# Optimization experiments

Hardware: AMD Instinct MI355X
Metric: run time of the kernel (lower is better)

The kernel has to match this reference:

```python
import jax, jax.numpy as jnp
import numpy as np

EPSILON = 1e-8
DT = 0.1
STEPS = 3
MASK_DENSITY = 0.01


def setup_inputs() -> dict:
    key = jax.random.key(0)
    k1, k2 = jax.random.split(key)
    B, S, D = 4, 4096, 2
    psi = jax.random.normal(k1, (B, S, D), dtype=jnp.float32)
    # binary mask: threshold a uniform draw to get a sparse 0/1 adjacency
    u = jax.random.uniform(k2, (B, S, S), dtype=jnp.float32)
    binary_mask = (u < MASK_DENSITY).astype(jnp.float32)
    return {"psi": psi, "binary_mask": binary_mask}


def reference(psi, binary_mask):
    def force(state):
        # adjacency-weighted aggregation minus self: [B,S,S] @ [B,S,2]
        return jnp.einsum('bij,bjd->bid', binary_mask, state) - state

    def step(p, _):
        r = jnp.linalg.norm(p, axis=-1, keepdims=True)          # [B,S,1]
        k1 = force(p)
        psi_star = p + DT * k1
        star_norm = jnp.linalg.norm(psi_star, axis=-1, keepdims=True)
        psi_star = psi_star * (r / (star_norm + EPSILON))       # renormalize to r
        k2 = force(psi_star)
        p_new = p + 0.5 * DT * (k1 + k2)
        new_norm = jnp.linalg.norm(p_new, axis=-1, keepdims=True)
        p_new = p_new * (r / (new_norm + EPSILON))              # norm-preserving
        return p_new, None

    psi_out, _ = jax.lax.scan(step, psi, None, length=STEPS)
    return psi_out
```

## Files before the change

kernel.cpp:

```cpp
#include <hip/hip_runtime.h>
#include <stdint.h>

#define BATCH   4
#define SEQ     4096
#define NROWS   (BATCH * SEQ)
#define SLOTS   80
#define SENT    SEQ
#define DTS     0.1f
#define HALF_DT 0.05f
#define EPS     1e-8f

#define NBLK    256
#define NTHR    1024

typedef float fx4 __attribute__((ext_vector_type(4)));

__device__ __forceinline__ float2 ballot_force_sum(unsigned long long w,
                                                   const float2* __restrict__ gb,
                                                   int lane) {
    const int colbase = ((lane >> 2) << 8) | (lane & 3);
    float sx = 0.f, sy = 0.f;
    while (w) {
        int j = __builtin_ctzll(w);
        w &= (w - 1);
        float2 v = gb[colbase + (j << 2)];
        sx += v.x; sy += v.y;
    }
#pragma unroll
    for (int m = 32; m >= 1; m >>= 1) {
        sx += __shfl_xor(sx, m, 64);
        sy += __shfl_xor(sy, m, 64);
    }
    return make_float2(sx, sy);
}

__global__ __launch_bounds__(256)
void compress_phaseA(const float* __restrict__ mask,
                     const float2* __restrict__ psi,
                     ushort* __restrict__ idx,
                     float2* __restrict__ k1buf,
                     float2* __restrict__ starbuf,
                     float*  __restrict__ rbuf) {
    const int row  = (blockIdx.x * blockDim.x + threadIdx.x) >> 6;
    const int lane = threadIdx.x & 63;

    const fx4* src = reinterpret_cast<const fx4*>(mask + (size_t)row * SEQ);
    unsigned long long word = 0ull;
#pragma unroll
    for (int c = 0; c < 16; ++c) {
        fx4 v = __builtin_nontemporal_load(&src[c * 64 + lane]);
        unsigned long long b;
        b = __ballot(v.x != 0.f); if (lane == c * 4 + 0) word = b;
        b = __ballot(v.y != 0.f); if (lane == c * 4 + 1) word = b;
        b = __ballot(v.z != 0.f); if (lane == c * 4 + 2) word = b;
        b = __ballot(v.w != 0.f); if (lane == c * 4 + 3) word = b;
    }

    int pc  = __popcll(word);
    int inc = pc;
#pragma unroll
    for (int ofs = 1; ofs < 64; ofs <<= 1) {
        int t = __shfl_up(inc, ofs, 64);
        if (lane >= ofs) inc += t;
    }
    int pos   = inc - pc;
    int total = __shfl(inc, 63, 64);

    ushort* dst = idx + (size_t)row * SLOTS;
    const int colbase = ((lane >> 2) << 8) | (lane & 3);
    unsigned long long w = word;
    while (w) {
        int j = __builtin_ctzll(w);
        w &= (w - 1);
        if (pos < SLOTS) dst[pos] = (ushort)(colbase + (j << 2));
        ++pos;
    }
    for (int s = total + lane; s < SLOTS; s += 64) dst[s] = (ushort)SENT;

    const int bidx = row >> 12;
    float2 sum = ballot_force_sum(word, psi + ((size_t)bidx << 12), lane);
    float2 p  = psi[row];
    float r   = sqrtf(p.x * p.x + p.y * p.y);
    float k1x = sum.x - p.x, k1y = sum.y - p.y;
    float tx  = p.x + DTS * k1x, ty = p.y + DTS * k1y;
    float sc  = r / (sqrtf(tx * tx + ty * ty) + EPS);
    if (lane == 0) {
        k1buf[row]   = make_float2(k1x, k1y);
        rbuf[row]    = r;
        starbuf[row] = make_float2(tx * sc, ty * sc);
    }
}

__device__ __forceinline__ void gbar(int* __restrict__ bar, int gen) {
    __syncthreads();
    if (threadIdx.x == 0) {
        __threadfence();
        atomicAdd(bar, 1);
        while (__hip_atomic_load(bar, __ATOMIC_RELAXED,
                                 __HIP_MEMORY_SCOPE_AGENT) < gen * NBLK)
            __builtin_amdgcn_s_sleep(2);
        __threadfence();
    }
    __syncthreads();
}

__global__ __launch_bounds__(NTHR)
void forces(const ushort* __restrict__ idx,
            const float2* __restrict__ psi,
            float2* __restrict__ pbuf,
            float2* __restrict__ star,
            float2* __restrict__ k1buf,
            float*  __restrict__ rbuf,
            float2* __restrict__ out,
            int*    __restrict__ bar) {
    __shared__ float2 SRC[SEQ + 2];

    const int t    = threadIdx.x;
    const int g    = t >> 4;
    const int q    = t & 15;
    const int row  = (blockIdx.x << 6) + g;
    const int bidx = row >> 12;
    const int rloc = row & 4095;
    const size_t bo = (size_t)bidx << 12;

    const ushort* __restrict__ ip = idx + (size_t)row * SLOTS;
    int c[5];
#pragma unroll
    for (int r = 0; r < 5; ++r) c[r] = ip[q * 5 + r];

    int gen = 0;
#pragma unroll 1
    for (int ph = 0; ph < 5; ++ph) {
        const bool isA = (ph & 1);
        const float2* __restrict__ gb = (isA ? pbuf : star) + bo;

        {
            const float4* __restrict__ s4 = reinterpret_cast<const float4*>(gb);
            float4* l4 = reinterpret_cast<float4*>(SRC);
            l4[t] = s4[t];
            l4[t + 1024] = s4[t + 1024];
            if (t == 0) SRC[SEQ] = make_float2(0.f, 0.f);
        }
        float2 p = make_float2(0.f, 0.f), k1 = make_float2(0.f, 0.f);
        float  rv = 0.f;
        if (!isA) {
            p  = (ph == 0) ? psi[row] : pbuf[row];
            k1 = k1buf[row];
            rv = rbuf[row];
        }
        __syncthreads();

        float sx = 0.f, sy = 0.f;
#pragma unroll
        for (int r = 0; r < 5; ++r) {
            float2 v = SRC[c[r]];
            sx += v.x; sy += v.y;
        }
#pragma unroll
        for (int m = 8; m >= 1; m >>= 1) {
            sx += __shfl_xor(sx, m, 64);
            sy += __shfl_xor(sy, m, 64);
        }

        if (q == 0) {
            if (isA) {
                float2 ps = SRC[rloc];
                float r   = sqrtf(ps.x * ps.x + ps.y * ps.y);
                float k1x = sx - ps.x, k1y = sy - ps.y;
                float tx  = ps.x + DTS * k1x, ty = ps.y + DTS * k1y;
                float sc  = r / (sqrtf(tx * tx + ty * ty) + EPS);
                k1buf[row] = make_float2(k1x, k1y);
                rbuf[row]  = r;
                star[row]  = make_float2(tx * sc, ty * sc);
            } else {
                float2 st = SRC[rloc];
                float k2x = sx - st.x, k2y = sy - st.y;
                float nx  = p.x + HALF_DT * (k1.x + k2x);
                float ny  = p.y + HALF_DT * (k1.y + k2y);
                float sc  = rv / (sqrtf(nx * nx + ny * ny) + EPS);
                float2 pn = make_float2(nx * sc, ny * sc);
                if (ph == 4) out[row]  = pn;
                else         pbuf[row] = pn;
            }
        }
        if (ph < 4) gbar(bar, ++gen);
    }
}

extern "C" void kernel_launch(void* const* d_in, const int* in_sizes, int n_in,
                              void* d_out, int out_size, void* d_ws, size_t ws_size,
                              hipStream_t stream) {
    const float* psi  = (const float*)d_in[0];
    const float* mask = (const float*)d_in[1];
    float2* out2 = (float2*)d_out;

    char* ws = (char*)d_ws;
    ushort* idx  = (ushort*)ws;
    float2* pbuf = (float2*)(ws + (size_t)NROWS * SLOTS * sizeof(ushort));
    float2* star = pbuf + NROWS;
    float2* k1   = star + NROWS;
    float*  rbuf = (float*)(k1 + NROWS);
    int*    bar  = (int*)(rbuf + NROWS);

    const float2* psi2 = (const float2*)psi;

    hipMemsetAsync(bar, 0, 64, stream);
    compress_phaseA<<<NROWS / 4, 256, 0, stream>>>(mask, psi2, idx, k1, star, rbuf);
    forces<<<NBLK, NTHR, 0, stream>>>(idx, psi2, pbuf, star, k1, rbuf, out2, bar);
}
```

Measured before the change: 406.9 us.

## Replace persistent grid-barrier kernel with per-phase kernel launches

Replaces the single persistent 256x1024 kernel that used a software grid barrier between five phases with five separate launches of a templated 256-thread kernel, each handling 64 rows (4 rows per 16-lane group). Stream ordering now provides the inter-phase sync instead of atomic spinning, and the barrier memset goes away. In exchange each launch pays launch overhead and reloads the 32KB gather source into LDS per block. Phase 1 reads and writes pbuf in place, which is safe because each row only reads and writes its own entry.

Result: faster. 356.5 us (-12.4%).

```diff
diff --git a/kernel.cpp b/kernel.cpp
--- a/kernel.cpp
+++ b/kernel.cpp
@@ -9,9 +9,6 @@
 #define DTS     0.1f
 #define HALF_DT 0.05f
 #define EPS     1e-8f
-
-#define NBLK    256
-#define NTHR    1024
 
 typedef float fx4 __attribute__((ext_vector_type(4)));
 
@@ -91,69 +88,59 @@
     }
 }
 
-__device__ __forceinline__ void gbar(int* __restrict__ bar, int gen) {
-    __syncthreads();
-    if (threadIdx.x == 0) {
-        __threadfence();
-        atomicAdd(bar, 1);
-        while (__hip_atomic_load(bar, __ATOMIC_RELAXED,
-                                 __HIP_MEMORY_SCOPE_AGENT) < gen * NBLK)
-            __builtin_amdgcn_s_sleep(2);
-        __threadfence();
-    }
-    __syncthreads();
-}
-
-__global__ __launch_bounds__(NTHR)
-void forces(const ushort* __restrict__ idx,
-            const float2* __restrict__ psi,
-            float2* __restrict__ pbuf,
-            float2* __restrict__ star,
-            float2* __restrict__ k1buf,
-            float*  __restrict__ rbuf,
-            float2* __restrict__ out,
-            int*    __restrict__ bar) {
+template <int PHASE>
+__global__ __launch_bounds__(256)
+void force_step(const ushort* __restrict__ idx,
+                const float2* __restrict__ pIn,
+                const float2* __restrict__ gath,
+                float2* __restrict__ k1buf,
+                float*  __restrict__ rbuf,
+                float2* __restrict__ outbuf) {
     __shared__ float2 SRC[SEQ + 2];
 
-    const int t    = threadIdx.x;
-    const int g    = t >> 4;
-    const int q    = t & 15;
-    const int row  = (blockIdx.x << 6) + g;
-    const int bidx = row >> 12;
-    const int rloc = row & 4095;
+    const int t     = threadIdx.x;
+    const int g     = t >> 4;
+    const int q     = t & 15;
+    const int row0  = (blockIdx.x << 6);
+    const int bidx  = row0 >> 12;
     const size_t bo = (size_t)bidx << 12;
+    const float2* __restrict__ gb = gath + bo;
 
-    const ushort* __restrict__ ip = idx + (size_t)row * SLOTS;
-    int c[5];
+    {
+        const float4* __restrict__ s4 = reinterpret_cast<const float4*>(gb);
+        float4* l4 = reinterpret_cast<float4*>(SRC);
 #pragma unroll
-    for (int r = 0; r < 5; ++r) c[r] = ip[q * 5 + r];
+        for (int k = 0; k < 8; ++k) l4[t + k * 256] = s4[t + k * 256];
+        if (t == 0) SRC[SEQ] = make_float2(0.f, 0.f);
+    }
 
-    int gen = 0;
-#pragma unroll 1
-    for (int ph = 0; ph < 5; ++ph) {
-        const bool isA = (ph & 1);
-        const float2* __restrict__ gb = (isA ? pbuf : star) + bo;
+    int c[4][5];
+    float2 p[4], k1[4];
+    float  rv[4];
+#pragma unroll
+    for (int rr = 0; rr < 4; ++rr) {
+        const int row = row0 + g + (rr << 4);
+        const ushort* __restrict__ ip = idx + (size_t)row * SLOTS;
+#pragma unroll
+        for (int r = 0; r < 5; ++r) c[rr][r] = ip[q * 5 + r];
+        if (PHASE == 1) {
+            p[rr]  = pIn[row];
+            k1[rr] = k1buf[row];
+            rv[rr] = rbuf[row];
+        }
+    }
 
-        {
-            const float4* __restrict__ s4 = reinterpret_cast<const float4*>(gb);
-            float4* l4 = reinterpret_cast<float4*>(SRC);
-            l4[t] = s4[t];
-            l4[t + 1024] = s4[t + 1024];
-            if (t == 0) SRC[SEQ] = make_float2(0.f, 0.f);
-        }
-        float2 p = make_float2(0.f, 0.f), k1 = make_float2(0.f, 0.f);
-        float  rv = 0.f;
-        if (!isA) {
-            p  = (ph == 0) ? psi[row] : pbuf[row];
-            k1 = k1buf[row];
-            rv = rbuf[row];
-        }
-        __syncthreads();
+    __syncthreads();
+
+#pragma unroll
+    for (int rr = 0; rr < 4; ++rr) {
+        const int row  = row0 + g + (rr << 4);
+        const int rloc = row & 4095;
 
         float sx = 0.f, sy = 0.f;
 #pragma unroll
         for (int r = 0; r < 5; ++r) {
-            float2 v = SRC[c[r]];
+            float2 v = SRC[c[rr][r]];
             sx += v.x; sy += v.y;
         }
 #pragma unroll
@@ -163,27 +150,24 @@
         }
 
         if (q == 0) {
-            if (isA) {
+            if (PHASE == 0) {
                 float2 ps = SRC[rloc];
                 float r   = sqrtf(ps.x * ps.x + ps.y * ps.y);
                 float k1x = sx - ps.x, k1y = sy - ps.y;
                 float tx  = ps.x + DTS * k1x, ty = ps.y + DTS * k1y;
                 float sc  = r / (sqrtf(tx * tx + ty * ty) + EPS);
-                k1buf[row] = make_float2(k1x, k1y);
-                rbuf[row]  = r;
-                star[row]  = make_float2(tx * sc, ty * sc);
+                k1buf[row]  = make_float2(k1x, k1y);
+                rbuf[row]   = r;
+                outbuf[row] = make_float2(tx * sc, ty * sc);
             } else {
                 float2 st = SRC[rloc];
                 float k2x = sx - st.x, k2y = sy - st.y;
-                float nx  = p.x + HALF_DT * (k1.x + k2x);
-                float ny  = p.y + HALF_DT * (k1.y + k2y);
-                float sc  = rv / (sqrtf(nx * nx + ny * ny) + EPS);
-                float2 pn = make_float2(nx * sc, ny * sc);
-                if (ph == 4) out[row]  = pn;
-                else         pbuf[row] = pn;
+                float nx  = p[rr].x + HALF_DT * (k1[rr].x + k2x);
+                float ny  = p[rr].y + HALF_DT * (k1[rr].y + k2y);
+                float sc  = rv[rr] / (sqrtf(nx * nx + ny * ny) + EPS);
+                outbuf[row] = make_float2(nx * sc, ny * sc);
             }
         }
-        if (ph < 4) gbar(bar, ++gen);
     }
 }
 
@@ -200,11 +184,14 @@
     float2* star = pbuf + NROWS;
     float2* k1   = star + NROWS;
     float*  rbuf = (float*)(k1 + NROWS);
-    int*    bar  = (int*)(rbuf + NROWS);
 
     const float2* psi2 = (const float2*)psi;
+    const int gridF = NROWS / 64;
 
-    hipMemsetAsync(bar, 0, 64, stream);
     compress_phaseA<<<NROWS / 4, 256, 0, stream>>>(mask, psi2, idx, k1, star, rbuf);
-    forces<<<NBLK, NTHR, 0, stream>>>(idx, psi2, pbuf, star, k1, rbuf, out2, bar);
+    force_step<1><<<gridF, 256, 0, stream>>>(idx, psi2, star, k1, rbuf, pbuf);
+    force_step<0><<<gridF, 256, 0, stream>>>(idx, nullptr, pbuf, k1, rbuf, star);
+    force_step<1><<<gridF, 256, 0, stream>>>(idx, pbuf, star, k1, rbuf, pbuf);
+    force_step<0><<<gridF, 256, 0, stream>>>(idx, nullptr, pbuf, k1, rbuf, star);
+    force_step<1><<<gridF, 256, 0, stream>>>(idx, pbuf, star, k1, rbuf, out2);
 }
```

## Shrink forces blocks to 256 threads and use relaxed-atomic fence-free grid barrier

Applied to the files above, without the earlier changes.

Rewrites the persistent forces kernel to use 256-thread blocks, each thread processing four rows, and replaces the fenced grid barrier with a relaxed atomic counter without threadfences. Cross-block shared state (star, pbuf) is now read and written through agent-scope relaxed atomic 64-bit loads and stores, so it stays coherent without full fences. The aim is to cut barrier cost between phases and reduce per-block overhead, at the risk of subtle memory-ordering issues and a longer per-thread LDS fill.

After: 376.8 us. 7.4% less time.

```diff
diff --git a/kernel.cpp b/kernel.cpp
--- a/kernel.cpp
+++ b/kernel.cpp
@@ -11,9 +11,31 @@
 #define EPS     1e-8f
 
 #define NBLK    256
-#define NTHR    1024
 
 typedef float fx4 __attribute__((ext_vector_type(4)));
+
+__device__ __forceinline__ float2 aload8(const float2* p) {
+    unsigned long long u = __hip_atomic_load(
+        reinterpret_cast<const unsigned long long*>(p),
+        __ATOMIC_RELAXED, __HIP_MEMORY_SCOPE_AGENT);
+    float2 f; __builtin_memcpy(&f, &u, 8); return f;
+}
+__device__ __forceinline__ void astore8(float2* p, float2 v) {
+    unsigned long long u; __builtin_memcpy(&u, &v, 8);
+    __hip_atomic_store(reinterpret_cast<unsigned long long*>(p), u,
+                       __ATOMIC_RELAXED, __HIP_MEMORY_SCOPE_AGENT);
+}
+
+__device__ __forceinline__ void gbar(int* bar, int target) {
+    __syncthreads();
+    if (threadIdx.x == 0) {
+        __hip_atomic_fetch_add(bar, 1, __ATOMIC_RELAXED, __HIP_MEMORY_SCOPE_AGENT);
+        while (__hip_atomic_load(bar, __ATOMIC_RELAXED,
+                                 __HIP_MEMORY_SCOPE_AGENT) < target)
+            __builtin_amdgcn_s_sleep(4);
+    }
+    __syncthreads();
+}
 
 __device__ __forceinline__ float2 ballot_force_sum(unsigned long long w,
                                                    const float2* __restrict__ gb,
@@ -91,20 +113,7 @@
     }
 }
 
-__device__ __forceinline__ void gbar(int* __restrict__ bar, int gen) {
-    __syncthreads();
-    if (threadIdx.x == 0) {
-        __threadfence();
-        atomicAdd(bar, 1);
-        while (__hip_atomic_load(bar, __ATOMIC_RELAXED,
-                                 __HIP_MEMORY_SCOPE_AGENT) < gen * NBLK)
-            __builtin_amdgcn_s_sleep(2);
-        __threadfence();
-    }
-    __syncthreads();
-}
-
-__global__ __launch_bounds__(NTHR)
+__global__ __launch_bounds__(256)
 void forces(const ushort* __restrict__ idx,
             const float2* __restrict__ psi,
             float2* __restrict__ pbuf,
@@ -118,72 +127,86 @@
     const int t    = threadIdx.x;
     const int g    = t >> 4;
     const int q    = t & 15;
-    const int row  = (blockIdx.x << 6) + g;
-    const int bidx = row >> 12;
-    const int rloc = row & 4095;
+    const int row0 = (blockIdx.x << 6);
+    const int bidx = row0 >> 12;
     const size_t bo = (size_t)bidx << 12;
 
-    const ushort* __restrict__ ip = idx + (size_t)row * SLOTS;
-    int c[5];
-#pragma unroll
-    for (int r = 0; r < 5; ++r) c[r] = ip[q * 5 + r];
-
-    int gen = 0;
+    int c[4][5];
+#pragma unroll
+    for (int rr = 0; rr < 4; ++rr) {
+        const int row = row0 + g + (rr << 4);
+        const ushort* __restrict__ ip = idx + (size_t)row * SLOTS;
+#pragma unroll
+        for (int r = 0; r < 5; ++r) c[rr][r] = ip[q * 5 + r];
+    }
+
 #pragma unroll 1
     for (int ph = 0; ph < 5; ++ph) {
         const bool isA = (ph & 1);
-        const float2* __restrict__ gb = (isA ? pbuf : star) + bo;
+        const float2* gbG = (isA ? pbuf : star) + bo;
 
         {
-            const float4* __restrict__ s4 = reinterpret_cast<const float4*>(gb);
-            float4* l4 = reinterpret_cast<float4*>(SRC);
-            l4[t] = s4[t];
-            l4[t + 1024] = s4[t + 1024];
+            float2 v[16];
+#pragma unroll
+            for (int k = 0; k < 16; ++k) v[k] = aload8(gbG + t + k * 256);
+#pragma unroll
+            for (int k = 0; k < 16; ++k) SRC[t + k * 256] = v[k];
             if (t == 0) SRC[SEQ] = make_float2(0.f, 0.f);
         }
-        float2 p = make_float2(0.f, 0.f), k1 = make_float2(0.f, 0.f);
-        float  rv = 0.f;
+
+        float2 p[4], k1v[4];
+        float  rv[4];
         if (!isA) {
-            p  = (ph == 0) ? psi[row] : pbuf[row];
-            k1 = k1buf[row];
-            rv = rbuf[row];
+#pragma unroll
+            for (int rr = 0; rr < 4; ++rr) {
+                const int row = row0 + g + (rr << 4);
+                p[rr]   = (ph == 0) ? psi[row] : aload8(&pbuf[row]);
+                k1v[rr] = k1buf[row];
+                rv[rr]  = rbuf[row];
+            }
         }
         __syncthreads();
 
-        float sx = 0.f, sy = 0.f;
-#pragma unroll
-        for (int r = 0; r < 5; ++r) {
-            float2 v = SRC[c[r]];
-            sx += v.x; sy += v.y;
+#pragma unroll
+        for (int rr = 0; rr < 4; ++rr) {
+            const int row  = row0 + g + (rr << 4);
+            const int rloc = row & 4095;
+
+            float sx = 0.f, sy = 0.f;
+#pragma unroll
+            for (int r = 0; r < 5; ++r) {
+                float2 v = SRC[c[rr][r]];
+                sx += v.x; sy += v.y;
+            }
+#pragma unroll
+            for (int m = 8; m >= 1; m >>= 1) {
+                sx += __shfl_xor(sx, m, 64);
+                sy += __shfl_xor(sy, m, 64);
+            }
+
+            if (q == 0) {
+                if (isA) {
+                    float2 ps = SRC[rloc];
+                    float r   = sqrtf(ps.x * ps.x + ps.y * ps.y);
+                    float k1x = sx - ps.x, k1y = sy - ps.y;
+                    float tx  = ps.x + DTS * k1x, ty = ps.y + DTS * k1y;
+                    float sc  = r / (sqrtf(tx * tx + ty * ty) + EPS);
+                    k1buf[row] = make_float2(k1x, k1y);
+                    rbuf[row]  = r;
+                    astore8(&star[row], make_float2(tx * sc, ty * sc));
+                } else {
+                    float2 st = SRC[rloc];
+                    float k2x = sx - st.x, k2y = sy - st.y;
+                    float nx  = p[rr].x + HALF_DT * (k1v[rr].x + k2x);
+                    float ny  = p[rr].y + HALF_DT * (k1v[rr].y + k2y);
+                    float sc  = rv[rr] / (sqrtf(nx * nx + ny * ny) + EPS);
+                    float2 pn = make_float2(nx * sc, ny * sc);
+                    if (ph == 4) out[row] = pn;
+                    else         astore8(&pbuf[row], pn);
+                }
+            }
         }
-#pragma unroll
-        for (int m = 8; m >= 1; m >>= 1) {
-            sx += __shfl_xor(sx, m, 64);
-            sy += __shfl_xor(sy, m, 64);
-        }
-
-        if (q == 0) {
-            if (isA) {
-                float2 ps = SRC[rloc];
-                float r   = sqrtf(ps.x * ps.x + ps.y * ps.y);
-                float k1x = sx - ps.x, k1y = sy - ps.y;
-                float tx  = ps.x + DTS * k1x, ty = ps.y + DTS * k1y;
-                float sc  = r / (sqrtf(tx * tx + ty * ty) + EPS);
-                k1buf[row] = make_float2(k1x, k1y);
-                rbuf[row]  = r;
-                star[row]  = make_float2(tx * sc, ty * sc);
-            } else {
-                float2 st = SRC[rloc];
-                float k2x = sx - st.x, k2y = sy - st.y;
-                float nx  = p.x + HALF_DT * (k1.x + k2x);
-                float ny  = p.y + HALF_DT * (k1.y + k2y);
-                float sc  = rv / (sqrtf(nx * nx + ny * ny) + EPS);
-                float2 pn = make_float2(nx * sc, ny * sc);
-                if (ph == 4) out[row]  = pn;
-                else         pbuf[row] = pn;
-            }
-        }
-        if (ph < 4) gbar(bar, ++gen);
+        if (ph < 4) gbar(bar, (ph + 1) * NBLK);
     }
 }
 
@@ -206,5 +229,5 @@
 
     hipMemsetAsync(bar, 0, 64, stream);
     compress_phaseA<<<NROWS / 4, 256, 0, stream>>>(mask, psi2, idx, k1, star, rbuf);
-    forces<<<NBLK, NTHR, 0, stream>>>(idx, psi2, pbuf, star, k1, rbuf, out2, bar);
-}
+    forces<<<NBLK, 256, 0, stream>>>(idx, psi2, pbuf, star, k1, rbuf, out2, bar);
+}
```
